# Optimization experiments

Hardware: AMD Instinct MI355X
Metric: run time of the kernel (lower is better)

The kernel has to match this reference:

```python
import jax, jax.numpy as jnp
import numpy as np

B, NH, T, D = 2, 16, 2048, 64

def setup_inputs() -> dict:
    key = jax.random.key(0)
    kq, kk, kv = jax.random.split(key, 3)
    Q = jax.random.normal(kq, (B, NH, T, D), dtype=jnp.float32)
    K = jax.random.normal(kk, (B, NH, T, D), dtype=jnp.float32)
    V = jax.random.normal(kv, (B, NH, T, D), dtype=jnp.float32)
    return {"Q": Q, "K": K, "V": V}

def reference(Q, K, V):
    # scores: [B, nh, T, T]
    Dh = Q.shape[-1]
    scale = 1.0 / jnp.sqrt(jnp.asarray(Dh, Q.dtype))
    scores = jnp.einsum('bhtd,bhsd->bhts', Q, K) * scale
    Tq = Q.shape[2]
    causal = jnp.tril(jnp.ones((Tq, Tq), dtype=bool))
    scores = jnp.where(causal, scores, jnp.asarray(-jnp.inf, scores.dtype))
    attn = jax.nn.softmax(scores, axis=-1)
    return jnp.einsum('bhts,bhsd->bhtd', attn, V)
```

## Files before the change

kernel.cpp:

```cpp
#include <hip/hip_runtime.h>
#include <hip/hip_bf16.h>


typedef __bf16 bf16;
typedef __bf16 bf16x4 __attribute__((ext_vector_type(4)));
typedef __bf16 bf16x8 __attribute__((ext_vector_type(8)));
typedef float floatx4 __attribute__((ext_vector_type(4)));

#define T_SEQ 2048
#define DH 64
#define TQ 128
#define TK 64
#define NQT (T_SEQ / TQ)
#define BHN 32
#define CEXP 0.18033688011112042f

__device__ __forceinline__ void gload16(const bf16* g, bf16* l) {
    __builtin_amdgcn_global_load_lds(
        (const __attribute__((address_space(1))) void*)g,
        (__attribute__((address_space(3))) void*)l, 16, 0, 0);
}

__global__ __launch_bounds__(256) void prep(const float* __restrict__ K,
                                            const float* __restrict__ V,
                                            bf16* __restrict__ Kb,
                                            bf16* __restrict__ Vt) {
    const int bid = (int)blockIdx.x;
    const int tid = (int)threadIdx.x;
    if (bid < 1024) {
        const size_t i = ((size_t)bid * 256 + tid) * 16;
        float4 a = *(const float4*)(K + i + 0);
        float4 b = *(const float4*)(K + i + 4);
        float4 c = *(const float4*)(K + i + 8);
        float4 d = *(const float4*)(K + i + 12);
        bf16x8 o0, o1;
        o0[0]=(bf16)a.x; o0[1]=(bf16)a.y; o0[2]=(bf16)a.z; o0[3]=(bf16)a.w;
        o0[4]=(bf16)b.x; o0[5]=(bf16)b.y; o0[6]=(bf16)b.z; o0[7]=(bf16)b.w;
        o1[0]=(bf16)c.x; o1[1]=(bf16)c.y; o1[2]=(bf16)c.z; o1[3]=(bf16)c.w;
        o1[4]=(bf16)d.x; o1[5]=(bf16)d.y; o1[6]=(bf16)d.z; o1[7]=(bf16)d.w;
        *(bf16x8*)(Kb + i + 0) = o0;
        *(bf16x8*)(Kb + i + 8) = o1;
        return;
    }
    __shared__ bf16 tile[64][72];
    const int vb = bid - 1024;
    const int bh = vb & (BHN - 1);
    const int t0 = (vb >> 5) * 64;
    {
        const int r = tid >> 2;
        const int c = (tid & 3) * 16;
        const float* s = V + ((size_t)bh * T_SEQ + t0 + r) * DH + c;
        float4 f0 = *(const float4*)(s + 0);
        float4 f1 = *(const float4*)(s + 4);
        float4 f2 = *(const float4*)(s + 8);
        float4 f3 = *(const float4*)(s + 12);
        bf16x8 p0, p1;
        p0[0]=(bf16)f0.x; p0[1]=(bf16)f0.y; p0[2]=(bf16)f0.z; p0[3]=(bf16)f0.w;
        p0[4]=(bf16)f1.x; p0[5]=(bf16)f1.y; p0[6]=(bf16)f1.z; p0[7]=(bf16)f1.w;
        p1[0]=(bf16)f2.x; p1[1]=(bf16)f2.y; p1[2]=(bf16)f2.z; p1[3]=(bf16)f2.w;
        p1[4]=(bf16)f3.x; p1[5]=(bf16)f3.y; p1[6]=(bf16)f3.z; p1[7]=(bf16)f3.w;
        *(bf16x8*)&tile[r][c + 0] = p0;
        *(bf16x8*)&tile[r][c + 8] = p1;
    }
    __syncthreads();
    {
        const int d   = tid >> 2;
        const int tch = (tid & 3) * 16;
        bf16x8 o0, o1;
        #pragma unroll
        for (int j = 0; j < 8; ++j) { o0[j] = tile[tch + j][d]; o1[j] = tile[tch + 8 + j][d]; }
        bf16* o = Vt + ((size_t)bh * DH + d) * T_SEQ + t0 + tch;
        *(bf16x8*)(o + 0) = o0;
        *(bf16x8*)(o + 8) = o1;
    }
}

__global__ __launch_bounds__(256, 2)
void fa_fwd(const float* __restrict__ Qg, const bf16* __restrict__ Kb,
            const bf16* __restrict__ Vt, float* __restrict__ Og)
{
    __shared__ __align__(16) bf16 Ksh[2][TK * DH];
    __shared__ __align__(16) bf16 Vsh[2][DH * TK];
    __shared__ __align__(16) bf16 Psh[4][32 * TK];

    const int gid  = (int)blockIdx.x;
    const int pair = gid & 255;
    const int half = gid >> 8;
    const int bh   = pair & (BHN - 1);
    const int ip   = pair >> 5;
    const int iq   = half ? ip : (NQT - 1 - ip);
    const int q0   = iq * TQ;
    const int nkt  = 2 * iq + 2;

    const int tid  = (int)threadIdx.x;
    const int wave = tid >> 6;
    const int lane = tid & 63;
    const int quad = lane >> 4;
    const int l16  = lane & 15;
    const int rl   = lane >> 3;
    const int gch  = (lane & 7) ^ rl;

    const bf16* Kbh = Kb + (size_t)bh * T_SEQ * DH;
    const bf16* Vbh = Vt + (size_t)bh * DH * T_SEQ;

    const int qw = q0 + wave * 32;

    bf16x8 qb[2][2];
    #pragma unroll
    for (int nt = 0; nt < 2; ++nt) {
        const int qrow = qw + nt * 16 + l16;
        #pragma unroll
        for (int kk = 0; kk < 2; ++kk) {
            const float* s = Qg + ((size_t)bh * T_SEQ + qrow) * DH + kk * 32 + quad * 8;
            float4 f0 = *(const float4*)(s);
            float4 f1 = *(const float4*)(s + 4);
            bf16x8 t;
            t[0]=(bf16)f0.x; t[1]=(bf16)f0.y; t[2]=(bf16)f0.z; t[3]=(bf16)f0.w;
            t[4]=(bf16)f1.x; t[5]=(bf16)f1.y; t[6]=(bf16)f1.z; t[7]=(bf16)f1.w;
            qb[nt][kk] = t;
        }
    }

    floatx4 oacc[4][2];
    #pragma unroll
    for (int mt = 0; mt < 4; ++mt)
        #pragma unroll
        for (int nt = 0; nt < 2; ++nt) oacc[mt][nt] = (floatx4){0.f,0.f,0.f,0.f};
    float lpart[2] = {0.f, 0.f};

    auto stage = [&](int kt, int buf) {
        const bf16* kg = Kbh + (size_t)kt * TK * DH;
        const bf16* vg = Vbh + kt * TK;
        #pragma unroll
        for (int g = 0; g < 2; ++g) {
            const int row = wave * 16 + g * 8;
            gload16(kg + (size_t)(row + rl) * DH + gch * 8, &Ksh[buf][row * DH]);
            gload16(vg + (size_t)(row + rl) * T_SEQ + gch * 8, &Vsh[buf][row * TK]);
        }
    };

    stage(0, 0);
    __syncthreads();

    for (int kt = 0; kt < nkt; ++kt) {
        const int buf = kt & 1;
        const int k0  = kt * TK;
        if (kt + 1 < nkt) stage(kt + 1, buf ^ 1);

        floatx4 sacc[4][2];
        #pragma unroll
        for (int mt = 0; mt < 4; ++mt)
            #pragma unroll
            for (int nt = 0; nt < 2; ++nt) sacc[mt][nt] = (floatx4){0.f,0.f,0.f,0.f};
        #pragma unroll
        for (int kk = 0; kk < 2; ++kk) {
            #pragma unroll
            for (int mt = 0; mt < 4; ++mt) {
                const int R = mt * 16 + l16;
                bf16x8 kf = *(const bf16x8*)&Ksh[buf][R * DH + (((kk * 4 + quad) ^ (l16 & 7)) * 8)];
                #pragma unroll
                for (int nt = 0; nt < 2; ++nt)
                    sacc[mt][nt] = __builtin_amdgcn_mfma_f32_16x16x32_bf16(kf, qb[nt][kk], sacc[mt][nt], 0, 0, 0);
            }
        }

        if (k0 + TK - 1 > qw) {
            #pragma unroll
            for (int mt = 0; mt < 4; ++mt) {
                #pragma unroll
                for (int nt = 0; nt < 2; ++nt) {
                    const int qg = qw + nt * 16 + l16;
                    #pragma unroll
                    for (int r = 0; r < 4; ++r) {
                        const int keyg = k0 + mt * 16 + quad * 4 + r;
                        if (keyg > qg) sacc[mt][nt][r] = -INFINITY;
                    }
                }
            }
        }

        bf16* Pw = Psh[wave];
        #pragma unroll
        for (int mt = 0; mt < 4; ++mt) {
            #pragma unroll
            for (int nt = 0; nt < 2; ++nt) {
                bf16x4 w;
                #pragma unroll
                for (int r = 0; r < 4; ++r) {
                    const float p = __builtin_amdgcn_exp2f(CEXP * sacc[mt][nt][r]);
                    lpart[nt] += p;
                    w[r] = (bf16)p;
                }
                const int row = nt * 16 + l16;
                const int c   = (mt * 2 + (quad >> 1)) ^ (row & 7);
                *(bf16x4*)&Pw[row * TK + c * 8 + (quad & 1) * 4] = w;
            }
        }

        bf16x8 pf[2][2];
        #pragma unroll
        for (int nt = 0; nt < 2; ++nt) {
            const int row = nt * 16 + l16;
            #pragma unroll
            for (int kk = 0; kk < 2; ++kk)
                pf[nt][kk] = *(const bf16x8*)&Pw[row * TK + (((kk * 4 + quad) ^ (row & 7)) * 8)];
        }

        #pragma unroll
        for (int kk = 0; kk < 2; ++kk) {
            #pragma unroll
            for (int mt = 0; mt < 4; ++mt) {
                const int R = mt * 16 + l16;
                bf16x8 vf = *(const bf16x8*)&Vsh[buf][R * TK + (((kk * 4 + quad) ^ (l16 & 7)) * 8)];
                #pragma unroll
                for (int nt = 0; nt < 2; ++nt)
                    oacc[mt][nt] = __builtin_amdgcn_mfma_f32_16x16x32_bf16(vf, pf[nt][kk], oacc[mt][nt], 0, 0, 0);
            }
        }

        __syncthreads();
    }

    float invl[2];
    #pragma unroll
    for (int nt = 0; nt < 2; ++nt) {
        float v = lpart[nt];
        v += __shfl_xor(v, 16);
        v += __shfl_xor(v, 32);
        invl[nt] = 1.0f / v;
    }

    #pragma unroll
    for (int nt = 0; nt < 2; ++nt) {
        const size_t qrow = (size_t)bh * T_SEQ + qw + nt * 16 + l16;
        #pragma unroll
        for (int mt = 0; mt < 4; ++mt) {
            float4 o;
            o.x = oacc[mt][nt][0] * invl[nt];
            o.y = oacc[mt][nt][1] * invl[nt];
            o.z = oacc[mt][nt][2] * invl[nt];
            o.w = oacc[mt][nt][3] * invl[nt];
            *(float4*)&Og[qrow * DH + mt * 16 + quad * 4] = o;
        }
    }
}

extern "C" void kernel_launch(void* const* d_in, const int* in_sizes, int n_in,
                              void* d_out, int out_size, void* d_ws, size_t ws_size,
                              hipStream_t stream) {
    const float* Q = (const float*)d_in[0];
    const float* K = (const float*)d_in[1];
    const float* V = (const float*)d_in[2];
    float* O = (float*)d_out;
    (void)in_sizes; (void)n_in; (void)out_size; (void)ws_size;

    const size_t nelem = (size_t)BHN * T_SEQ * DH;
    bf16* Kbf = (bf16*)d_ws;
    bf16* Vtb = Kbf + nelem;

    prep<<<dim3(2048), dim3(256), 0, stream>>>(K, V, Kbf, Vtb);
    fa_fwd<<<dim3(512), dim3(256), 0, stream>>>(Q, Kbf, Vtb, O);
}
```

Before: 137.8 us.

## Split causal KV range across blocks with atomic partial accumulation and normalize pass

Replaces one-block-per-query-tile scheduling with a table-driven split-KV scheme: long query tiles are split into chunks of at most eight KV tiles spread over 1280 blocks, and partial unnormalized outputs and row sums are accumulated into zeroed fp32 buffers via atomicAdd. A new norm kernel transposes and divides by the row sum. The aim is better load balance and occupancy across CUs. In exchange it drops LDS double buffering, adds many scattered atomics, and adds an extra zeroing pass and a third kernel. It appears to rely on the softmax using a fixed max-free exponent so that partials can be summed directly.

```diff
diff --git a/kernel.cpp b/kernel.cpp
--- a/kernel.cpp
+++ b/kernel.cpp
@@ -11,7 +11,6 @@
 #define DH 64
 #define TQ 128
 #define TK 64
-#define NQT (T_SEQ / TQ)
 #define BHN 32
 #define CEXP 0.18033688011112042f
 
@@ -21,12 +20,34 @@
         (__attribute__((address_space(3))) void*)l, 16, 0, 0);
 }
 
+__device__ __constant__ unsigned char iq_tab[40] = {
+    15,15,15,15, 14,14,14, 13,13,13, 12,12,12, 11,11,11,
+    10,10, 9,9, 8,8, 7,7, 6,5,4,3,
+    14,10,6,2, 12,8,4,0, 13,9,5,1};
+__device__ __constant__ unsigned char k0_tab[40] = {
+    0,8,16,24, 0,8,16, 0,8,16, 0,8,16, 0,8,16,
+    0,8, 0,8, 0,8, 0,8, 0,0,0,0,
+    24,16,8,0, 24,16,8,0, 24,16,8,0};
+__device__ __constant__ unsigned char len_tab[40] = {
+    8,8,8,8,8,8,8,8,8,8,8,8,8,8,8,8,8,8,8,8,8,8,8,8,8,8,8,8,
+    6,6,6,6, 2,2,2,2, 4,4,4,4};
+
 __global__ __launch_bounds__(256) void prep(const float* __restrict__ K,
                                             const float* __restrict__ V,
                                             bf16* __restrict__ Kb,
-                                            bf16* __restrict__ Vt) {
+                                            bf16* __restrict__ Vt,
+                                            float* __restrict__ Zb) {
     const int bid = (int)blockIdx.x;
     const int tid = (int)threadIdx.x;
+    if (bid >= 2048) {
+        const size_t idx = ((size_t)(bid - 2048) * 1024 + tid * 4) * 4;
+        float4 z = {0.f, 0.f, 0.f, 0.f};
+        *(float4*)(Zb + idx + 0)  = z;
+        *(float4*)(Zb + idx + 4)  = z;
+        *(float4*)(Zb + idx + 8)  = z;
+        *(float4*)(Zb + idx + 12) = z;
+        return;
+    }
     if (bid < 1024) {
         const size_t i = ((size_t)bid * 256 + tid) * 16;
         float4 a = *(const float4*)(K + i + 0);
@@ -75,22 +96,22 @@
     }
 }
 
-__global__ __launch_bounds__(256, 2)
+__global__ __launch_bounds__(256, 5)
 void fa_fwd(const float* __restrict__ Qg, const bf16* __restrict__ Kb,
-            const bf16* __restrict__ Vt, float* __restrict__ Og)
+            const bf16* __restrict__ Vt, float* __restrict__ On,
+            float* __restrict__ Ls)
 {
-    __shared__ __align__(16) bf16 Ksh[2][TK * DH];
-    __shared__ __align__(16) bf16 Vsh[2][DH * TK];
+    __shared__ __align__(16) bf16 Ksh[TK * DH];
+    __shared__ __align__(16) bf16 Vsh[DH * TK];
     __shared__ __align__(16) bf16 Psh[4][32 * TK];
 
-    const int gid  = (int)blockIdx.x;
-    const int pair = gid & 255;
-    const int half = gid >> 8;
-    const int bh   = pair & (BHN - 1);
-    const int ip   = pair >> 5;
-    const int iq   = half ? ip : (NQT - 1 - ip);
-    const int q0   = iq * TQ;
-    const int nkt  = 2 * iq + 2;
+    const int gid = (int)blockIdx.x;
+    const int r_  = gid >> 5;
+    const int bh  = gid & (BHN - 1);
+    const int iq  = iq_tab[r_];
+    const int kt0 = k0_tab[r_];
+    const int nk  = len_tab[r_];
+    const int q0  = iq * TQ;
 
     const int tid  = (int)threadIdx.x;
     const int wave = tid >> 6;
@@ -102,7 +123,6 @@
 
     const bf16* Kbh = Kb + (size_t)bh * T_SEQ * DH;
     const bf16* Vbh = Vt + (size_t)bh * DH * T_SEQ;
-
     const int qw = q0 + wave * 32;
 
     bf16x8 qb[2][2];
@@ -128,24 +148,20 @@
         for (int nt = 0; nt < 2; ++nt) oacc[mt][nt] = (floatx4){0.f,0.f,0.f,0.f};
     float lpart[2] = {0.f, 0.f};
 
-    auto stage = [&](int kt, int buf) {
-        const bf16* kg = Kbh + (size_t)kt * TK * DH;
-        const bf16* vg = Vbh + kt * TK;
-        #pragma unroll
-        for (int g = 0; g < 2; ++g) {
-            const int row = wave * 16 + g * 8;
-            gload16(kg + (size_t)(row + rl) * DH + gch * 8, &Ksh[buf][row * DH]);
-            gload16(vg + (size_t)(row + rl) * T_SEQ + gch * 8, &Vsh[buf][row * TK]);
-        }
-    };
-
-    stage(0, 0);
-    __syncthreads();
-
-    for (int kt = 0; kt < nkt; ++kt) {
-        const int buf = kt & 1;
-        const int k0  = kt * TK;
-        if (kt + 1 < nkt) stage(kt + 1, buf ^ 1);
+    for (int it = 0; it < nk; ++it) {
+        const int kt = kt0 + it;
+        const int k0 = kt * TK;
+        {
+            const bf16* kg = Kbh + (size_t)kt * TK * DH;
+            const bf16* vg = Vbh + kt * TK;
+            #pragma unroll
+            for (int g = 0; g < 2; ++g) {
+                const int row = wave * 16 + g * 8;
+                gload16(kg + (size_t)(row + rl) * DH + gch * 8, &Ksh[row * DH]);
+                gload16(vg + (size_t)(row + rl) * T_SEQ + gch * 8, &Vsh[row * TK]);
+            }
+        }
+        __syncthreads();
 
         floatx4 sacc[4][2];
         #pragma unroll
@@ -157,7 +173,7 @@
             #pragma unroll
             for (int mt = 0; mt < 4; ++mt) {
                 const int R = mt * 16 + l16;
-                bf16x8 kf = *(const bf16x8*)&Ksh[buf][R * DH + (((kk * 4 + quad) ^ (l16 & 7)) * 8)];
+                bf16x8 kf = *(const bf16x8*)&Ksh[R * DH + (((kk * 4 + quad) ^ (l16 & 7)) * 8)];
                 #pragma unroll
                 for (int nt = 0; nt < 2; ++nt)
                     sacc[mt][nt] = __builtin_amdgcn_mfma_f32_16x16x32_bf16(kf, qb[nt][kk], sacc[mt][nt], 0, 0, 0);
@@ -211,7 +227,7 @@
             #pragma unroll
             for (int mt = 0; mt < 4; ++mt) {
                 const int R = mt * 16 + l16;
-                bf16x8 vf = *(const bf16x8*)&Vsh[buf][R * TK + (((kk * 4 + quad) ^ (l16 & 7)) * 8)];
+                bf16x8 vf = *(const bf16x8*)&Vsh[R * TK + (((kk * 4 + quad) ^ (l16 & 7)) * 8)];
                 #pragma unroll
                 for (int nt = 0; nt < 2; ++nt)
                     oacc[mt][nt] = __builtin_amdgcn_mfma_f32_16x16x32_bf16(vf, pf[nt][kk], oacc[mt][nt], 0, 0, 0);
@@ -221,26 +237,58 @@
         __syncthreads();
     }
 
-    float invl[2];
     #pragma unroll
     for (int nt = 0; nt < 2; ++nt) {
         float v = lpart[nt];
         v += __shfl_xor(v, 16);
         v += __shfl_xor(v, 32);
-        invl[nt] = 1.0f / v;
-    }
-
-    #pragma unroll
-    for (int nt = 0; nt < 2; ++nt) {
-        const size_t qrow = (size_t)bh * T_SEQ + qw + nt * 16 + l16;
+        const int qglob = qw + nt * 16 + l16;
+        if (quad == 0) atomicAdd(&Ls[(size_t)bh * T_SEQ + qglob], v);
         #pragma unroll
         for (int mt = 0; mt < 4; ++mt) {
+            #pragma unroll
+            for (int r = 0; r < 4; ++r) {
+                const int d = mt * 16 + quad * 4 + r;
+                atomicAdd(&On[((size_t)bh * DH + d) * T_SEQ + qglob], oacc[mt][nt][r]);
+            }
+        }
+    }
+}
+
+__global__ __launch_bounds__(256) void norm(const float* __restrict__ On,
+                                            const float* __restrict__ Ls,
+                                            float* __restrict__ O) {
+    __shared__ float tile[64][65];
+    const int bh = (int)blockIdx.x & (BHN - 1);
+    const int t0 = ((int)blockIdx.x >> 5) * 64;
+    const int tid = (int)threadIdx.x;
+    {
+        const int r = tid >> 2;
+        const int c = (tid & 3) * 16;
+        const float* s = On + ((size_t)bh * DH + r) * T_SEQ + t0 + c;
+        #pragma unroll
+        for (int g = 0; g < 4; ++g) {
+            float4 f = *(const float4*)(s + g * 4);
+            tile[r][c + g * 4 + 0] = f.x;
+            tile[r][c + g * 4 + 1] = f.y;
+            tile[r][c + g * 4 + 2] = f.z;
+            tile[r][c + g * 4 + 3] = f.w;
+        }
+    }
+    __syncthreads();
+    {
+        const int q  = tid >> 2;
+        const int dc = (tid & 3) * 16;
+        const float linv = 1.0f / Ls[(size_t)bh * T_SEQ + t0 + q];
+        float* dst = O + ((size_t)bh * T_SEQ + t0 + q) * DH + dc;
+        #pragma unroll
+        for (int g = 0; g < 4; ++g) {
             float4 o;
-            o.x = oacc[mt][nt][0] * invl[nt];
-            o.y = oacc[mt][nt][1] * invl[nt];
-            o.z = oacc[mt][nt][2] * invl[nt];
-            o.w = oacc[mt][nt][3] * invl[nt];
-            *(float4*)&Og[qrow * DH + mt * 16 + quad * 4] = o;
+            o.x = tile[dc + g * 4 + 0][q] * linv;
+            o.y = tile[dc + g * 4 + 1][q] * linv;
+            o.z = tile[dc + g * 4 + 2][q] * linv;
+            o.w = tile[dc + g * 4 + 3][q] * linv;
+            *(float4*)(dst + g * 4) = o;
         }
     }
 }
@@ -255,9 +303,12 @@
     (void)in_sizes; (void)n_in; (void)out_size; (void)ws_size;
 
     const size_t nelem = (size_t)BHN * T_SEQ * DH;
-    bf16* Kbf = (bf16*)d_ws;
-    bf16* Vtb = Kbf + nelem;
-
-    prep<<<dim3(2048), dim3(256), 0, stream>>>(K, V, Kbf, Vtb);
-    fa_fwd<<<dim3(512), dim3(256), 0, stream>>>(Q, Kbf, Vtb, O);
-}
+    bf16*  Kbf = (bf16*)d_ws;
+    bf16*  Vtb = Kbf + nelem;
+    float* On  = (float*)(Vtb + nelem);
+    float* Ls  = On + nelem;
+
+    prep<<<dim3(3088), dim3(256), 0, stream>>>(K, V, Kbf, Vtb, On);
+    fa_fwd<<<dim3(1280), dim3(256), 0, stream>>>(Q, Kbf, Vtb, On, Ls);
+    norm<<<dim3(1024), dim3(256), 0, stream>>>(On, Ls, O);
+}
```

Result: slower. 206.6 us (+50.0%).

## Split key loop across two wave groups per block and reduce partials in LDS

Applied to the files above, without the earlier changes.

Doubles the block to 8 waves, with two groups of four waves each handling alternating key tiles for the same 128 query rows. The partial output accumulators and row sums are combined through shared memory at the end. Cross-iteration prefetch double buffering is replaced by a load-then-sync per step, and score computation is fused per tile with masking and exponentiation. The aim is more parallelism and latency hiding per CU. The cost is lost load/compute overlap, an extra reduction, and register pressure from the higher launch bounds.

```diff
diff --git a/kernel.cpp b/kernel.cpp
--- a/kernel.cpp
+++ b/kernel.cpp
@@ -75,35 +75,38 @@
     }
 }
 
-__global__ __launch_bounds__(256, 2)
+__global__ __launch_bounds__(512, 4)
 void fa_fwd(const float* __restrict__ Qg, const bf16* __restrict__ Kb,
             const bf16* __restrict__ Vt, float* __restrict__ Og)
 {
-    __shared__ __align__(16) bf16 Ksh[2][TK * DH];
-    __shared__ __align__(16) bf16 Vsh[2][DH * TK];
-    __shared__ __align__(16) bf16 Psh[4][32 * TK];
+    __shared__ __align__(16) bf16 smem[32768];
 
     const int gid  = (int)blockIdx.x;
-    const int pair = gid & 255;
     const int half = gid >> 8;
-    const int bh   = pair & (BHN - 1);
-    const int ip   = pair >> 5;
-    const int iq   = half ? ip : (NQT - 1 - ip);
+    const int idx  = gid & 255;
+    const int bh   = idx & (BHN - 1);
+    const int p_   = idx >> 5;
+    const int iq   = half ? p_ : (NQT - 1 - p_);
     const int q0   = iq * TQ;
-    const int nkt  = 2 * iq + 2;
+    const int nsteps = iq + 1;
 
     const int tid  = (int)threadIdx.x;
     const int wave = tid >> 6;
+    const int w4   = wave & 3;
+    const int g2   = wave >> 2;
     const int lane = tid & 63;
     const int quad = lane >> 4;
     const int l16  = lane & 15;
     const int rl   = lane >> 3;
     const int gch  = (lane & 7) ^ rl;
 
+    bf16* Ksh = smem + g2 * 4096;
+    bf16* Vsh = smem + 8192 + g2 * 4096;
+    bf16* Pw  = smem + 16384 + wave * 2048;
+
     const bf16* Kbh = Kb + (size_t)bh * T_SEQ * DH;
     const bf16* Vbh = Vt + (size_t)bh * DH * T_SEQ;
-
-    const int qw = q0 + wave * 32;
+    const int qw = q0 + w4 * 32;
 
     bf16x8 qb[2][2];
     #pragma unroll
@@ -128,90 +131,72 @@
         for (int nt = 0; nt < 2; ++nt) oacc[mt][nt] = (floatx4){0.f,0.f,0.f,0.f};
     float lpart[2] = {0.f, 0.f};
 
-    auto stage = [&](int kt, int buf) {
-        const bf16* kg = Kbh + (size_t)kt * TK * DH;
-        const bf16* vg = Vbh + kt * TK;
-        #pragma unroll
-        for (int g = 0; g < 2; ++g) {
-            const int row = wave * 16 + g * 8;
-            gload16(kg + (size_t)(row + rl) * DH + gch * 8, &Ksh[buf][row * DH]);
-            gload16(vg + (size_t)(row + rl) * T_SEQ + gch * 8, &Vsh[buf][row * TK]);
-        }
-    };
-
-    stage(0, 0);
-    __syncthreads();
-
-    for (int kt = 0; kt < nkt; ++kt) {
-        const int buf = kt & 1;
-        const int k0  = kt * TK;
-        if (kt + 1 < nkt) stage(kt + 1, buf ^ 1);
-
-        floatx4 sacc[4][2];
-        #pragma unroll
-        for (int mt = 0; mt < 4; ++mt)
-            #pragma unroll
-            for (int nt = 0; nt < 2; ++nt) sacc[mt][nt] = (floatx4){0.f,0.f,0.f,0.f};
+    for (int s = 0; s < nsteps; ++s) {
+        const int kt = 2 * s + g2;
+        const int k0 = kt * TK;
+        {
+            const bf16* kg = Kbh + (size_t)kt * TK * DH;
+            const bf16* vg = Vbh + kt * TK;
+            #pragma unroll
+            for (int g = 0; g < 2; ++g) {
+                const int row = w4 * 16 + g * 8;
+                gload16(kg + (size_t)(row + rl) * DH + gch * 8, &Ksh[row * DH]);
+                gload16(vg + (size_t)(row + rl) * T_SEQ + gch * 8, &Vsh[row * TK]);
+            }
+        }
+        __syncthreads();
+
+        const bool domask = (k0 + TK - 1 > qw);
+
+        #pragma unroll
+        for (int mt = 0; mt < 4; ++mt) {
+            floatx4 s0 = (floatx4){0.f,0.f,0.f,0.f};
+            floatx4 s1 = (floatx4){0.f,0.f,0.f,0.f};
+            const int R = mt * 16 + l16;
+            #pragma unroll
+            for (int kk = 0; kk < 2; ++kk) {
+                bf16x8 kf = *(const bf16x8*)&Ksh[R * DH + (((kk * 4 + quad) ^ (l16 & 7)) * 8)];
+                s0 = __builtin_amdgcn_mfma_f32_16x16x32_bf16(kf, qb[0][kk], s0, 0, 0, 0);
+                s1 = __builtin_amdgcn_mfma_f32_16x16x32_bf16(kf, qb[1][kk], s1, 0, 0, 0);
+            }
+            if (domask) {
+                #pragma unroll
+                for (int r = 0; r < 4; ++r) {
+                    const int keyg = k0 + mt * 16 + quad * 4 + r;
+                    if (keyg > qw + l16)      s0[r] = -INFINITY;
+                    if (keyg > qw + 16 + l16) s1[r] = -INFINITY;
+                }
+            }
+            bf16x4 w0, w1;
+            #pragma unroll
+            for (int r = 0; r < 4; ++r) {
+                const float p0 = __builtin_amdgcn_exp2f(CEXP * s0[r]);
+                const float p1 = __builtin_amdgcn_exp2f(CEXP * s1[r]);
+                lpart[0] += p0; lpart[1] += p1;
+                w0[r] = (bf16)p0; w1[r] = (bf16)p1;
+            }
+            const int c0 = (mt * 2 + (quad >> 1)) ^ (l16 & 7);
+            const int r1 = 16 + l16;
+            const int c1 = (mt * 2 + (quad >> 1)) ^ (r1 & 7);
+            *(bf16x4*)&Pw[l16 * TK + c0 * 8 + (quad & 1) * 4] = w0;
+            *(bf16x4*)&Pw[r1  * TK + c1 * 8 + (quad & 1) * 4] = w1;
+        }
+
+        bf16x8 pf[2][2];
+        #pragma unroll
+        for (int nt = 0; nt < 2; ++nt) {
+            const int row = nt * 16 + l16;
+            #pragma unroll
+            for (int kk = 0; kk < 2; ++kk)
+                pf[nt][kk] = *(const bf16x8*)&Pw[row * TK + (((kk * 4 + quad) ^ (row & 7)) * 8)];
+        }
+
         #pragma unroll
         for (int kk = 0; kk < 2; ++kk) {
             #pragma unroll
             for (int mt = 0; mt < 4; ++mt) {
                 const int R = mt * 16 + l16;
-                bf16x8 kf = *(const bf16x8*)&Ksh[buf][R * DH + (((kk * 4 + quad) ^ (l16 & 7)) * 8)];
-                #pragma unroll
-                for (int nt = 0; nt < 2; ++nt)
-                    sacc[mt][nt] = __builtin_amdgcn_mfma_f32_16x16x32_bf16(kf, qb[nt][kk], sacc[mt][nt], 0, 0, 0);
-            }
-        }
-
-        if (k0 + TK - 1 > qw) {
-            #pragma unroll
-            for (int mt = 0; mt < 4; ++mt) {
-                #pragma unroll
-                for (int nt = 0; nt < 2; ++nt) {
-                    const int qg = qw + nt * 16 + l16;
-                    #pragma unroll
-                    for (int r = 0; r < 4; ++r) {
-                        const int keyg = k0 + mt * 16 + quad * 4 + r;
-                        if (keyg > qg) sacc[mt][nt][r] = -INFINITY;
-                    }
-                }
-            }
-        }
-
-        bf16* Pw = Psh[wave];
-        #pragma unroll
-        for (int mt = 0; mt < 4; ++mt) {
-            #pragma unroll
-            for (int nt = 0; nt < 2; ++nt) {
-                bf16x4 w;
-                #pragma unroll
-                for (int r = 0; r < 4; ++r) {
-                    const float p = __builtin_amdgcn_exp2f(CEXP * sacc[mt][nt][r]);
-                    lpart[nt] += p;
-                    w[r] = (bf16)p;
-                }
-                const int row = nt * 16 + l16;
-                const int c   = (mt * 2 + (quad >> 1)) ^ (row & 7);
-                *(bf16x4*)&Pw[row * TK + c * 8 + (quad & 1) * 4] = w;
-            }
-        }
-
-        bf16x8 pf[2][2];
-        #pragma unroll
-        for (int nt = 0; nt < 2; ++nt) {
-            const int row = nt * 16 + l16;
-            #pragma unroll
-            for (int kk = 0; kk < 2; ++kk)
-                pf[nt][kk] = *(const bf16x8*)&Pw[row * TK + (((kk * 4 + quad) ^ (row & 7)) * 8)];
-        }
-
-        #pragma unroll
-        for (int kk = 0; kk < 2; ++kk) {
-            #pragma unroll
-            for (int mt = 0; mt < 4; ++mt) {
-                const int R = mt * 16 + l16;
-                bf16x8 vf = *(const bf16x8*)&Vsh[buf][R * TK + (((kk * 4 + quad) ^ (l16 & 7)) * 8)];
+                bf16x8 vf = *(const bf16x8*)&Vsh[R * TK + (((kk * 4 + quad) ^ (l16 & 7)) * 8)];
                 #pragma unroll
                 for (int nt = 0; nt < 2; ++nt)
                     oacc[mt][nt] = __builtin_amdgcn_mfma_f32_16x16x32_bf16(vf, pf[nt][kk], oacc[mt][nt], 0, 0, 0);
@@ -221,26 +206,42 @@
         __syncthreads();
     }
 
-    float invl[2];
-    #pragma unroll
-    for (int nt = 0; nt < 2; ++nt) {
-        float v = lpart[nt];
-        v += __shfl_xor(v, 16);
-        v += __shfl_xor(v, 32);
-        invl[nt] = 1.0f / v;
-    }
-
-    #pragma unroll
-    for (int nt = 0; nt < 2; ++nt) {
-        const size_t qrow = (size_t)bh * T_SEQ + qw + nt * 16 + l16;
-        #pragma unroll
-        for (int mt = 0; mt < 4; ++mt) {
-            float4 o;
-            o.x = oacc[mt][nt][0] * invl[nt];
-            o.y = oacc[mt][nt][1] * invl[nt];
-            o.z = oacc[mt][nt][2] * invl[nt];
-            o.w = oacc[mt][nt][3] * invl[nt];
-            *(float4*)&Og[qrow * DH + mt * 16 + quad * 4] = o;
+    float* cb = (float*)smem + w4 * 2048;
+    float* lb = (float*)(smem + 16384) + w4 * 128;
+    if (g2 == 1) {
+        #pragma unroll
+        for (int mt = 0; mt < 4; ++mt)
+            #pragma unroll
+            for (int nt = 0; nt < 2; ++nt)
+                *(floatx4*)&cb[((mt * 2 + nt) * 64 + lane) * 4] = oacc[mt][nt];
+        lb[lane * 2 + 0] = lpart[0];
+        lb[lane * 2 + 1] = lpart[1];
+    }
+    __syncthreads();
+    if (g2 == 0) {
+        lpart[0] += lb[lane * 2 + 0];
+        lpart[1] += lb[lane * 2 + 1];
+        float invl[2];
+        #pragma unroll
+        for (int nt = 0; nt < 2; ++nt) {
+            float v = lpart[nt];
+            v += __shfl_xor(v, 16);
+            v += __shfl_xor(v, 32);
+            invl[nt] = 1.0f / v;
+        }
+        #pragma unroll
+        for (int nt = 0; nt < 2; ++nt) {
+            const size_t qrow = (size_t)bh * T_SEQ + qw + nt * 16 + l16;
+            #pragma unroll
+            for (int mt = 0; mt < 4; ++mt) {
+                floatx4 ob = *(const floatx4*)&cb[((mt * 2 + nt) * 64 + lane) * 4];
+                float4 o;
+                o.x = (oacc[mt][nt][0] + ob[0]) * invl[nt];
+                o.y = (oacc[mt][nt][1] + ob[1]) * invl[nt];
+                o.z = (oacc[mt][nt][2] + ob[2]) * invl[nt];
+                o.w = (oacc[mt][nt][3] + ob[3]) * invl[nt];
+                *(float4*)&Og[qrow * DH + mt * 16 + quad * 4] = o;
+            }
         }
     }
 }
@@ -259,5 +260,5 @@
     bf16* Vtb = Kbf + nelem;
 
     prep<<<dim3(2048), dim3(256), 0, stream>>>(K, V, Kbf, Vtb);
-    fa_fwd<<<dim3(512), dim3(256), 0, stream>>>(Q, Kbf, Vtb, O);
-}
+    fa_fwd<<<dim3(512), dim3(512), 0, stream>>>(Q, Kbf, Vtb, O);
+}
```

Result: faster. 126.5 us (-8.1%).

## Split key range across four wave groups per heavy/light query-tile pair

Applied to the files above, without the earlier changes.

Each 1024-thread block now handles a balanced pair of query tiles (a heavy one and its mirror light one) and splits the combined 68 key tiles of 32 keys across four wave groups. Each group processes 17 steps, switching from the heavy to the light tile mid-stream and parking its heavy partial accumulator in bf16 registers. Partial outputs and row sums are then reduced across the groups through shared memory in serialized rounds. The intent is to balance causal work across blocks and shorten each block's critical path. In exchange it adds reduction and synchronization overhead, bf16 rounding of parked partial outputs, and a single-buffered K/V load with a barrier on every step.

```diff
diff --git a/kernel.cpp b/kernel.cpp
--- a/kernel.cpp
+++ b/kernel.cpp
@@ -10,8 +10,7 @@
 #define T_SEQ 2048
 #define DH 64
 #define TQ 128
-#define TK 64
-#define NQT (T_SEQ / TQ)
+#define TKS 32
 #define BHN 32
 #define CEXP 0.18033688011112042f
 
@@ -75,51 +74,59 @@
     }
 }
 
-__global__ __launch_bounds__(256, 2)
+__global__ __launch_bounds__(1024, 4)
 void fa_fwd(const float* __restrict__ Qg, const bf16* __restrict__ Kb,
             const bf16* __restrict__ Vt, float* __restrict__ Og)
 {
-    __shared__ __align__(16) bf16 Ksh[2][TK * DH];
-    __shared__ __align__(16) bf16 Vsh[2][DH * TK];
-    __shared__ __align__(16) bf16 Psh[4][32 * TK];
-
-    const int gid  = (int)blockIdx.x;
-    const int pair = gid & 255;
-    const int half = gid >> 8;
-    const int bh   = pair & (BHN - 1);
-    const int ip   = pair >> 5;
-    const int iq   = half ? ip : (NQT - 1 - ip);
-    const int q0   = iq * TQ;
-    const int nkt  = 2 * iq + 2;
+    __shared__ __align__(16) bf16 smem[32768];
+
+    const int bid = (int)blockIdx.x;
+    const int bh  = bid & (BHN - 1);
+    const int p   = bid >> 5;
+    const int q0h = (15 - p) * TQ;
+    const int q0l = p * TQ;
+    const int A   = 64 - 4 * p;
 
     const int tid  = (int)threadIdx.x;
     const int wave = tid >> 6;
+    const int w4   = wave & 3;
+    const int g2   = wave >> 2;
     const int lane = tid & 63;
     const int quad = lane >> 4;
     const int l16  = lane & 15;
     const int rl   = lane >> 3;
-    const int gch  = (lane & 7) ^ rl;
-
-    const bf16* Kbh = Kb + (size_t)bh * T_SEQ * DH;
-    const bf16* Vbh = Vt + (size_t)bh * DH * T_SEQ;
-
-    const int qw = q0 + wave * 32;
+    const int ch   = lane & 7;
+
+    bf16* Ksh = smem + g2 * 2048;
+    bf16* Vsh = smem + 8192 + g2 * 2048;
+    bf16* Pw  = smem + 16384 + wave * 1024;
+
+    const bf16* Kbh = Kb + (size_t)bh * (T_SEQ * DH);
+    const bf16* Vbh = Vt + (size_t)bh * (DH * T_SEQ);
+    const size_t qrb = (size_t)bh * T_SEQ;
+
+    const int t0 = g2 * 17;
+    bool isLight = (t0 >= A);
+    int qw = (isLight ? q0l : q0h) + w4 * 32;
 
     bf16x8 qb[2][2];
-    #pragma unroll
-    for (int nt = 0; nt < 2; ++nt) {
-        const int qrow = qw + nt * 16 + l16;
-        #pragma unroll
-        for (int kk = 0; kk < 2; ++kk) {
-            const float* s = Qg + ((size_t)bh * T_SEQ + qrow) * DH + kk * 32 + quad * 8;
-            float4 f0 = *(const float4*)(s);
-            float4 f1 = *(const float4*)(s + 4);
-            bf16x8 t;
-            t[0]=(bf16)f0.x; t[1]=(bf16)f0.y; t[2]=(bf16)f0.z; t[3]=(bf16)f0.w;
-            t[4]=(bf16)f1.x; t[5]=(bf16)f1.y; t[6]=(bf16)f1.z; t[7]=(bf16)f1.w;
-            qb[nt][kk] = t;
-        }
-    }
+    auto loadQ = [&](int qbase) {
+        #pragma unroll
+        for (int nt = 0; nt < 2; ++nt) {
+            const int qrow = qbase + w4 * 32 + nt * 16 + l16;
+            #pragma unroll
+            for (int kk = 0; kk < 2; ++kk) {
+                const float* s = Qg + (qrb + qrow) * DH + kk * 32 + quad * 8;
+                float4 f0 = *(const float4*)(s);
+                float4 f1 = *(const float4*)(s + 4);
+                bf16x8 t;
+                t[0]=(bf16)f0.x; t[1]=(bf16)f0.y; t[2]=(bf16)f0.z; t[3]=(bf16)f0.w;
+                t[4]=(bf16)f1.x; t[5]=(bf16)f1.y; t[6]=(bf16)f1.z; t[7]=(bf16)f1.w;
+                qb[nt][kk] = t;
+            }
+        }
+    };
+    loadQ(isLight ? q0l : q0h);
 
     floatx4 oacc[4][2];
     #pragma unroll
@@ -127,120 +134,193 @@
         #pragma unroll
         for (int nt = 0; nt < 2; ++nt) oacc[mt][nt] = (floatx4){0.f,0.f,0.f,0.f};
     float lpart[2] = {0.f, 0.f};
-
-    auto stage = [&](int kt, int buf) {
-        const bf16* kg = Kbh + (size_t)kt * TK * DH;
-        const bf16* vg = Vbh + kt * TK;
-        #pragma unroll
-        for (int g = 0; g < 2; ++g) {
-            const int row = wave * 16 + g * 8;
-            gload16(kg + (size_t)(row + rl) * DH + gch * 8, &Ksh[buf][row * DH]);
-            gload16(vg + (size_t)(row + rl) * T_SEQ + gch * 8, &Vsh[buf][row * TK]);
-        }
-    };
-
-    stage(0, 0);
-    __syncthreads();
-
-    for (int kt = 0; kt < nkt; ++kt) {
-        const int buf = kt & 1;
-        const int k0  = kt * TK;
-        if (kt + 1 < nkt) stage(kt + 1, buf ^ 1);
-
-        floatx4 sacc[4][2];
-        #pragma unroll
-        for (int mt = 0; mt < 4; ++mt)
-            #pragma unroll
-            for (int nt = 0; nt < 2; ++nt) sacc[mt][nt] = (floatx4){0.f,0.f,0.f,0.f};
+    bf16x4 parked[8];
+    #pragma unroll
+    for (int f = 0; f < 8; ++f) parked[f] = (bf16x4){(bf16)0.f,(bf16)0.f,(bf16)0.f,(bf16)0.f};
+    float lparkH[2] = {0.f, 0.f};
+
+    const int srow = w4 * 8 + rl;
+    const int sgch = ch ^ (srow & 7);
+    const int vd   = srow * 2 + (sgch >> 2);
+    const int vkc  = sgch & 3;
+
+    for (int s = 0; s < 17; ++s) {
+        const int t = t0 + s;
+        if (!isLight && t >= A) {
+            #pragma unroll
+            for (int f = 0; f < 8; ++f) {
+                bf16x4 w;
+                #pragma unroll
+                for (int e = 0; e < 4; ++e) w[e] = (bf16)oacc[f >> 1][f & 1][e];
+                parked[f] = w;
+            }
+            lparkH[0] = lpart[0]; lparkH[1] = lpart[1];
+            lpart[0] = lpart[1] = 0.f;
+            #pragma unroll
+            for (int mt = 0; mt < 4; ++mt)
+                #pragma unroll
+                for (int nt = 0; nt < 2; ++nt) oacc[mt][nt] = (floatx4){0.f,0.f,0.f,0.f};
+            isLight = true;
+            qw = q0l + w4 * 32;
+            loadQ(q0l);
+        }
+        const int kt = isLight ? (t - A) : t;
+        const int k0 = kt * TKS;
+
+        gload16(Kbh + (size_t)(k0 + srow) * DH + sgch * 8, &Ksh[w4 * 512]);
+        gload16(Vbh + (size_t)vd * T_SEQ + k0 + vkc * 8, &Vsh[w4 * 512]);
+        __syncthreads();
+
+        floatx4 sa[2][2];
+        #pragma unroll
+        for (int mt = 0; mt < 2; ++mt)
+            #pragma unroll
+            for (int nt = 0; nt < 2; ++nt) sa[mt][nt] = (floatx4){0.f,0.f,0.f,0.f};
         #pragma unroll
         for (int kk = 0; kk < 2; ++kk) {
             #pragma unroll
-            for (int mt = 0; mt < 4; ++mt) {
+            for (int mt = 0; mt < 2; ++mt) {
                 const int R = mt * 16 + l16;
-                bf16x8 kf = *(const bf16x8*)&Ksh[buf][R * DH + (((kk * 4 + quad) ^ (l16 & 7)) * 8)];
-                #pragma unroll
-                for (int nt = 0; nt < 2; ++nt)
-                    sacc[mt][nt] = __builtin_amdgcn_mfma_f32_16x16x32_bf16(kf, qb[nt][kk], sacc[mt][nt], 0, 0, 0);
-            }
-        }
-
-        if (k0 + TK - 1 > qw) {
-            #pragma unroll
-            for (int mt = 0; mt < 4; ++mt) {
+                bf16x8 kf = *(const bf16x8*)&Ksh[R * 64 + (((kk * 4 + quad) ^ (R & 7)) * 8)];
+                sa[mt][0] = __builtin_amdgcn_mfma_f32_16x16x32_bf16(kf, qb[0][kk], sa[mt][0], 0, 0, 0);
+                sa[mt][1] = __builtin_amdgcn_mfma_f32_16x16x32_bf16(kf, qb[1][kk], sa[mt][1], 0, 0, 0);
+            }
+        }
+        if (k0 + TKS - 1 > qw) {
+            #pragma unroll
+            for (int mt = 0; mt < 2; ++mt)
                 #pragma unroll
                 for (int nt = 0; nt < 2; ++nt) {
                     const int qg = qw + nt * 16 + l16;
                     #pragma unroll
                     for (int r = 0; r < 4; ++r) {
                         const int keyg = k0 + mt * 16 + quad * 4 + r;
-                        if (keyg > qg) sacc[mt][nt][r] = -INFINITY;
+                        if (keyg > qg) sa[mt][nt][r] = -INFINITY;
                     }
                 }
-            }
-        }
-
-        bf16* Pw = Psh[wave];
-        #pragma unroll
-        for (int mt = 0; mt < 4; ++mt) {
+        }
+        #pragma unroll
+        for (int mt = 0; mt < 2; ++mt)
             #pragma unroll
             for (int nt = 0; nt < 2; ++nt) {
                 bf16x4 w;
                 #pragma unroll
                 for (int r = 0; r < 4; ++r) {
-                    const float p = __builtin_amdgcn_exp2f(CEXP * sacc[mt][nt][r]);
-                    lpart[nt] += p;
-                    w[r] = (bf16)p;
+                    const float pv = __builtin_amdgcn_exp2f(CEXP * sa[mt][nt][r]);
+                    lpart[nt] += pv;
+                    w[r] = (bf16)pv;
                 }
-                const int row = nt * 16 + l16;
-                const int c   = (mt * 2 + (quad >> 1)) ^ (row & 7);
-                *(bf16x4*)&Pw[row * TK + c * 8 + (quad & 1) * 4] = w;
-            }
-        }
-
-        bf16x8 pf[2][2];
+                const int prow = nt * 8 + (l16 >> 1);
+                const int slot = ((l16 & 1) * 4 + mt * 2 + (quad >> 1)) ^ (prow & 7);
+                *(bf16x4*)&Pw[prow * 64 + slot * 8 + (quad & 1) * 4] = w;
+            }
+        bf16x8 pf[2];
         #pragma unroll
         for (int nt = 0; nt < 2; ++nt) {
-            const int row = nt * 16 + l16;
-            #pragma unroll
-            for (int kk = 0; kk < 2; ++kk)
-                pf[nt][kk] = *(const bf16x8*)&Pw[row * TK + (((kk * 4 + quad) ^ (row & 7)) * 8)];
-        }
-
-        #pragma unroll
-        for (int kk = 0; kk < 2; ++kk) {
-            #pragma unroll
-            for (int mt = 0; mt < 4; ++mt) {
-                const int R = mt * 16 + l16;
-                bf16x8 vf = *(const bf16x8*)&Vsh[buf][R * TK + (((kk * 4 + quad) ^ (l16 & 7)) * 8)];
-                #pragma unroll
-                for (int nt = 0; nt < 2; ++nt)
-                    oacc[mt][nt] = __builtin_amdgcn_mfma_f32_16x16x32_bf16(vf, pf[nt][kk], oacc[mt][nt], 0, 0, 0);
-            }
-        }
-
+            const int prow = nt * 8 + (l16 >> 1);
+            const int slot = ((l16 & 1) * 4 + quad) ^ (prow & 7);
+            pf[nt] = *(const bf16x8*)&Pw[prow * 64 + slot * 8];
+        }
+        #pragma unroll
+        for (int mt = 0; mt < 4; ++mt) {
+            const int vrow = mt * 8 + (l16 >> 1);
+            const int slot = ((l16 & 1) * 4 + quad) ^ (vrow & 7);
+            bf16x8 vf = *(const bf16x8*)&Vsh[vrow * 64 + slot * 8];
+            oacc[mt][0] = __builtin_amdgcn_mfma_f32_16x16x32_bf16(vf, pf[0], oacc[mt][0], 0, 0, 0);
+            oacc[mt][1] = __builtin_amdgcn_mfma_f32_16x16x32_bf16(vf, pf[1], oacc[mt][1], 0, 0, 0);
+        }
         __syncthreads();
     }
 
-    float invl[2];
-    #pragma unroll
-    for (int nt = 0; nt < 2; ++nt) {
-        float v = lpart[nt];
-        v += __shfl_xor(v, 16);
-        v += __shfl_xor(v, 32);
-        invl[nt] = 1.0f / v;
-    }
-
-    #pragma unroll
-    for (int nt = 0; nt < 2; ++nt) {
-        const size_t qrow = (size_t)bh * T_SEQ + qw + nt * 16 + l16;
-        #pragma unroll
-        for (int mt = 0; mt < 4; ++mt) {
+    float* LB = (float*)smem;
+    float* CB = (float*)smem + 1024;
+
+    const float hLs[2] = { isLight ? lparkH[0] : lpart[0], isLight ? lparkH[1] : lpart[1] };
+    const float lLs[2] = { isLight ? lpart[0] : 0.f,       isLight ? lpart[1] : 0.f };
+
+    for (int r = 0; r < 4; ++r) {
+        if (g2 == r) {
+            #pragma unroll
+            for (int nt = 0; nt < 2; ++nt) {
+                const int ih = ((0 * 4 + w4) * 2 + nt) * 64 + lane;
+                const int il = ((1 * 4 + w4) * 2 + nt) * 64 + lane;
+                LB[ih] = (r == 0) ? hLs[nt] : (LB[ih] + hLs[nt]);
+                LB[il] = (r == 0) ? lLs[nt] : (LB[il] + lLs[nt]);
+            }
+            float* base = CB + w4 * 2048;
+            #pragma unroll
+            for (int f = 0; f < 8; ++f) {
+                floatx4* a = (floatx4*)&base[(f * 64 + lane) * 4];
+                floatx4 v;
+                if (isLight) {
+                    v = (floatx4){(float)parked[f][0], (float)parked[f][1],
+                                  (float)parked[f][2], (float)parked[f][3]};
+                } else {
+                    v = oacc[f >> 1][f & 1];
+                }
+                if (r) v += *a;
+                *a = v;
+            }
+        }
+        __syncthreads();
+    }
+
+    if (g2 == 0) {
+        float invl[2];
+        #pragma unroll
+        for (int nt = 0; nt < 2; ++nt) {
+            float sl = 0.f;
+            #pragma unroll
+            for (int qd = 0; qd < 4; ++qd)
+                sl += LB[((0 * 4 + w4) * 2 + nt) * 64 + qd * 16 + l16];
+            invl[nt] = 1.0f / sl;
+        }
+        float* base = CB + w4 * 2048;
+        #pragma unroll
+        for (int f = 0; f < 8; ++f) {
+            floatx4 v = *(const floatx4*)&base[(f * 64 + lane) * 4];
+            const int nt = f & 1, mt = f >> 1;
             float4 o;
-            o.x = oacc[mt][nt][0] * invl[nt];
-            o.y = oacc[mt][nt][1] * invl[nt];
-            o.z = oacc[mt][nt][2] * invl[nt];
-            o.w = oacc[mt][nt][3] * invl[nt];
-            *(float4*)&Og[qrow * DH + mt * 16 + quad * 4] = o;
+            o.x = v[0] * invl[nt]; o.y = v[1] * invl[nt];
+            o.z = v[2] * invl[nt]; o.w = v[3] * invl[nt];
+            *(float4*)&Og[(qrb + q0h + w4 * 32 + nt * 16 + l16) * DH + mt * 16 + quad * 4] = o;
+        }
+    }
+    __syncthreads();
+
+    for (int r = 0; r < 4; ++r) {
+        if (g2 == r) {
+            float* base = CB + w4 * 2048;
+            #pragma unroll
+            for (int f = 0; f < 8; ++f) {
+                floatx4* a = (floatx4*)&base[(f * 64 + lane) * 4];
+                floatx4 v = isLight ? oacc[f >> 1][f & 1] : (floatx4){0.f,0.f,0.f,0.f};
+                if (r) v += *a;
+                *a = v;
+            }
+        }
+        __syncthreads();
+    }
+
+    if (g2 == 1) {
+        float invl[2];
+        #pragma unroll
+        for (int nt = 0; nt < 2; ++nt) {
+            float sl = 0.f;
+            #pragma unroll
+            for (int qd = 0; qd < 4; ++qd)
+                sl += LB[((1 * 4 + w4) * 2 + nt) * 64 + qd * 16 + l16];
+            invl[nt] = 1.0f / sl;
+        }
+        float* base = CB + w4 * 2048;
+        #pragma unroll
+        for (int f = 0; f < 8; ++f) {
+            floatx4 v = *(const floatx4*)&base[(f * 64 + lane) * 4];
+            const int nt = f & 1, mt = f >> 1;
+            float4 o;
+            o.x = v[0] * invl[nt]; o.y = v[1] * invl[nt];
+            o.z = v[2] * invl[nt]; o.w = v[3] * invl[nt];
+            *(float4*)&Og[(qrb + q0l + w4 * 32 + nt * 16 + l16) * DH + mt * 16 + quad * 4] = o;
         }
     }
 }
@@ -259,5 +339,5 @@
     bf16* Vtb = Kbf + nelem;
 
     prep<<<dim3(2048), dim3(256), 0, stream>>>(K, V, Kbf, Vtb);
-    fa_fwd<<<dim3(512), dim3(256), 0, stream>>>(Q, Kbf, Vtb, O);
+    fa_fwd<<<dim3(256), dim3(1024), 0, stream>>>(Q, Kbf, Vtb, O);
 }
```

New measurement: 131.2 us. 4.8% less time.
